# Performance work log

Hardware: AMD Instinct MI355X
Metric: run time of the kernel (lower is better)

Reference implementation:

```python
import jax, jax.numpy as jnp
import numpy as np

ALPHA = 0.1
B = 500_000
EMBED = 64
HIDDEN = 128
IN_DIM = 27 + 3 + EMBED  # 94

def _gelu(x):
    return jax.nn.gelu(x, approximate=False)  # torch.nn.GELU default = exact erf

def setup_inputs() -> dict:
    key = jax.random.key(0)
    ks = jax.random.split(key, 8)
    s = 0.05
    return {
        "F": jnp.eye(3, dtype=jnp.float32)[None] + 0.1 * jax.random.normal(ks[0], (B, 3, 3), jnp.float32),
        "latent_weight": jax.random.normal(ks[1], (1024, EMBED), jnp.float32),
        "W1": s * jax.random.normal(ks[2], (IN_DIM, HIDDEN), jnp.float32), "b1": jnp.zeros((HIDDEN,), jnp.float32),
        "W2": s * jax.random.normal(ks[3], (HIDDEN, HIDDEN), jnp.float32), "b2": jnp.zeros((HIDDEN,), jnp.float32),
        "W3": s * jax.random.normal(ks[4], (HIDDEN, HIDDEN), jnp.float32), "b3": jnp.zeros((HIDDEN,), jnp.float32),
        "W4": s * jax.random.normal(ks[5], (HIDDEN, HIDDEN), jnp.float32), "b4": jnp.zeros((HIDDEN,), jnp.float32),
        "W5": s * jax.random.normal(ks[6], (HIDDEN, 9), jnp.float32), "b5": jnp.zeros((9,), jnp.float32),
        "traj_ids": jnp.asarray(7, dtype=jnp.int32),
    }

def reference(F, latent_weight, W1, b1, W2, b2, W3, b3, W4, b4, W5, b5, traj_ids):
    n = F.shape[0]
    # Batched 3x3 SVD: F = U diag(s) Vh  (torch.svd returns V; Vh = V^T here)
    U, sigma, Vh = jnp.linalg.svd(F, full_matrices=False)
    R = jnp.matmul(U, Vh)  # [n,3,3] rotation
    lat = jnp.broadcast_to(latent_weight[traj_ids][None, :], (n, latent_weight.shape[1]))
    inv = jnp.concatenate(
        [F.reshape(n, 9), U.reshape(n, 9), sigma, Vh.reshape(n, 9), lat], axis=1)  # [n, 30+embed]
    h = _gelu(inv @ W1 + b1)
    h = _gelu(h @ W2 + b2)
    h = _gelu(h @ W3 + b3)
    h = _gelu(h @ W4 + b4)
    x = (h @ W5 + b5).reshape(n, 3, 3)
    x = 0.5 * (x + jnp.swapaxes(x, 1, 2))  # symmetrize
    return ALPHA * jnp.matmul(R, x) + F
```

## Files before the change

kernel.cpp:

```cpp
#include <hip/hip_runtime.h>


typedef short bf16x8 __attribute__((ext_vector_type(8)));
typedef float f32x4 __attribute__((ext_vector_type(4)));
typedef float f32x2 __attribute__((ext_vector_type(2)));
typedef unsigned int u32x2 __attribute__((ext_vector_type(2)));
typedef unsigned short u16;

#define WS_L1     0
#define WS_L234   8192
#define WS_L5     106496
#define WS_B1EFF  110592
#define WS_B234   111104
#define WS_B5     112640
#define WS_NEEDED 131072

__device__ __forceinline__ float bf2f(u16 b){
  union { unsigned int u; float f; } v; v.u = ((unsigned int)b) << 16; return v.f;
}
__device__ __forceinline__ u16 f2bf(float f){
  union { float f; unsigned int u; } v; v.f = f;
  unsigned int x = v.u;
  return (u16)((x + 0x7fffu + ((x >> 16) & 1u)) >> 16);
}
__device__ __forceinline__ unsigned int pack2bf(float f0, float f1){
  union { float f; unsigned int u; } a, b; a.f = f0; b.f = f1;
  unsigned int u0 = a.u + 0x8000u;
  unsigned int u1 = b.u + 0x8000u;
#if __has_builtin(__builtin_amdgcn_perm)
  return __builtin_amdgcn_perm(u1, u0, 0x07060302u);
#else
  return (u0 >> 16) | (u1 & 0xffff0000u);
#endif
}
template<bool B16>
__device__ __forceinline__ float ldf(const void* p, int i){
  return B16 ? bf2f(((const u16*)p)[i]) : ((const float*)p)[i];
}
template<bool B16>
__device__ __forceinline__ short ldw(const void* p, int i){
  return B16 ? (short)((const u16*)p)[i] : (short)f2bf(((const float*)p)[i]);
}
template<bool B16>
__device__ __forceinline__ void stf(void* p, int i, float v){
  if (B16) ((u16*)p)[i] = f2bf(v); else ((float*)p)[i] = v;
}

__device__ __forceinline__ float med3f(float x, float lo, float hi){
#if __has_builtin(__builtin_amdgcn_fmed3f)
  return __builtin_amdgcn_fmed3f(x, lo, hi);
#else
  return fminf(fmaxf(x, lo), hi);
#endif
}

__device__ __forceinline__ unsigned int gelu2_pack(float x0, float x1){
  const f32x2 A7 = {-2.20713e-4f, -2.20713e-4f};
  const f32x2 A5 = { 5.86695e-3f,  5.86695e-3f};
  const f32x2 A3 = {-5.99485e-2f, -5.99485e-2f};
  const f32x2 A1 = { 3.969014e-1f, 3.969014e-1f};
  const f32x2 HF = { 0.5f, 0.5f};
  f32x2 xc; xc[0] = med3f(x0, -3.4f, 3.4f); xc[1] = med3f(x1, -3.4f, 3.4f);
  f32x2 s  = xc * xc;
  f32x2 g  = s * A7 + A5;
  g = s * g + A3;
  g = s * g + A1;
  f32x2 ph = xc * g + HF;
  f32x2 xin; xin[0] = x0; xin[1] = x1;
  f32x2 y = xin * ph;
  return pack2bf(y[0], y[1]);
}

__device__ __forceinline__ int sniff_bf16(const void* Fg){
  const u16* fu = (const u16*)Fg;
  int votes = 0;
  #pragma unroll
  for (int k = 0; k < 32; ++k){
    u16 h = fu[k*18];
    votes += (h >= 0x3E00 && h < 0x4000) ? 1 : 0;
  }
  return votes >= 16;
}

template<int P, int Q, int R3>
__device__ __forceinline__ void jrot(float bm[3][3], float v[3][3]){
  float bpq = bm[P][Q];
  if (fabsf(bpq) < 1e-30f) return;
  float th = (bm[Q][Q] - bm[P][P]) / (2.0f * bpq);
  float t = copysignf(1.0f, th) / (fabsf(th) + sqrtf(1.0f + th*th));
  float c = 1.0f / sqrtf(1.0f + t*t);
  float s = t * c;
  float bpp = bm[P][P] - t*bpq;
  float bqq = bm[Q][Q] + t*bpq;
  bm[P][P] = bpp; bm[Q][Q] = bqq; bm[P][Q] = 0.0f; bm[Q][P] = 0.0f;
  float bpr = bm[P][R3], bqr = bm[Q][R3];
  float npr = c*bpr - s*bqr;
  float nqr = s*bpr + c*bqr;
  bm[P][R3] = npr; bm[R3][P] = npr;
  bm[Q][R3] = nqr; bm[R3][Q] = nqr;
  #pragma unroll
  for (int i = 0; i < 3; ++i){
    float vp = v[i][P], vq = v[i][Q];
    v[i][P] = c*vp - s*vq;
    v[i][Q] = s*vp + c*vq;
  }
}

__device__ __forceinline__ void svd3(const float Fm[9],
                                     float u[3][3], float sg[3], float vt[3][3]){
  float bm[3][3];
  #pragma unroll
  for (int i = 0; i < 3; ++i)
    #pragma unroll
    for (int j = i; j < 3; ++j){
      float acc = Fm[0*3+i]*Fm[0*3+j] + Fm[1*3+i]*Fm[1*3+j] + Fm[2*3+i]*Fm[2*3+j];
      bm[i][j] = acc; bm[j][i] = acc;
    }
  float v[3][3] = {{1.f,0.f,0.f},{0.f,1.f,0.f},{0.f,0.f,1.f}};
  #pragma unroll
  for (int sweep = 0; sweep < 5; ++sweep){
    jrot<0,1,2>(bm, v);
    jrot<0,2,1>(bm, v);
    jrot<1,2,0>(bm, v);
  }
  float lam0 = bm[0][0], lam1 = bm[1][1], lam2 = bm[2][2];
  #define CSWAP(la, lb, A, Bc) if ((la) < (lb)) { float t_ = la; la = lb; lb = t_; \
    for (int i_ = 0; i_ < 3; ++i_){ float w_ = v[i_][A]; v[i_][A] = v[i_][Bc]; v[i_][Bc] = w_; } }
  CSWAP(lam0, lam1, 0, 1);
  CSWAP(lam0, lam2, 0, 2);
  CSWAP(lam1, lam2, 1, 2);
  #undef CSWAP
  float a[3][3];
  #pragma unroll
  for (int c = 0; c < 3; ++c)
    #pragma unroll
    for (int r = 0; r < 3; ++r)
      a[r][c] = Fm[r*3+0]*v[0][c] + Fm[r*3+1]*v[1][c] + Fm[r*3+2]*v[2][c];
  float s1 = sqrtf(a[0][0]*a[0][0] + a[1][0]*a[1][0] + a[2][0]*a[2][0]);
  float inv1 = 1.0f / fmaxf(s1, 1e-30f);
  u[0][0] = a[0][0]*inv1; u[1][0] = a[1][0]*inv1; u[2][0] = a[2][0]*inv1;
  float d12 = u[0][0]*a[0][1] + u[1][0]*a[1][1] + u[2][0]*a[2][1];
  float w20 = a[0][1] - d12*u[0][0], w21 = a[1][1] - d12*u[1][0], w22 = a[2][1] - d12*u[2][0];
  float s2 = sqrtf(w20*w20 + w21*w21 + w22*w22);
  float inv2 = 1.0f / fmaxf(s2, 1e-30f);
  u[0][1] = w20*inv2; u[1][1] = w21*inv2; u[2][1] = w22*inv2;
  float d13 = u[0][0]*a[0][2] + u[1][0]*a[1][2] + u[2][0]*a[2][2];
  float d23 = u[0][1]*a[0][2] + u[1][1]*a[1][2] + u[2][1]*a[2][2];
  float w30 = a[0][2] - d13*u[0][0] - d23*u[0][1];
  float w31 = a[1][2] - d13*u[1][0] - d23*u[1][1];
  float w32 = a[2][2] - d13*u[2][0] - d23*u[2][1];
  float s3 = sqrtf(w30*w30 + w31*w31 + w32*w32);
  if (s3 > 1e-12f){
    float inv3 = 1.0f / s3;
    u[0][2] = w30*inv3; u[1][2] = w31*inv3; u[2][2] = w32*inv3;
  } else {
    float c0 = u[1][0]*u[2][1] - u[2][0]*u[1][1];
    float c1 = u[2][0]*u[0][1] - u[0][0]*u[2][1];
    float c2 = u[0][0]*u[1][1] - u[1][0]*u[0][1];
    float dt = c0*a[0][2] + c1*a[1][2] + c2*a[2][2];
    float sgn = (dt < 0.0f) ? -1.0f : 1.0f;
    u[0][2] = c0*sgn; u[1][2] = c1*sgn; u[2][2] = c2*sgn;
    s3 = fabsf(dt);
  }
  sg[0] = s1; sg[1] = s2; sg[2] = s3;
  #pragma unroll
  for (int i = 0; i < 3; ++i)
    #pragma unroll
    for (int j = 0; j < 3; ++j)
      vt[i][j] = v[j][i];
}

template<bool B16>
__device__ void prep_body(
  const void* latg, const void* w1g, const void* b1g,
  const void* w2g, const void* b2g, const void* w3g, const void* b3g,
  const void* w4g, const void* b4g, const void* w5g, const void* b5g,
  const int* trajg, char* ws)
{
  const int tid = threadIdx.x, lane = tid & 63, wv = tid >> 6;
  const int quad = lane >> 4, l15 = lane & 15;
  const int blk = blockIdx.x;
  if (blk < 27){
    const int wr = blk*4 + wv;
    bf16x8 frag;
    if (wr < 8){
      const int ntg = wr;
      #pragma unroll
      for (int j = 0; j < 8; ++j)
        frag[j] = ldw<B16>(w1g, (quad*8 + j)*128 + ntg*16 + l15);
      *(bf16x8*)(ws + WS_L1 + (size_t)(wr*64 + lane)*16) = frag;
    } else if (wr < 104){
      const int idx = wr - 8, layer = idx >> 5, rem = idx & 31;
      const int ntg = rem >> 2, ks = rem & 3;
      const void* wg = (layer == 0) ? w2g : ((layer == 1) ? w3g : w4g);
      #pragma unroll
      for (int j = 0; j < 8; ++j)
        frag[j] = ldw<B16>(wg, (ks*32 + quad*8 + j)*128 + ntg*16 + l15);
      *(bf16x8*)(ws + WS_L234 + (size_t)(idx*64 + lane)*16) = frag;
    } else {
      const int ks = wr - 104;
      #pragma unroll
      for (int j = 0; j < 8; ++j)
        frag[j] = (l15 < 9) ? ldw<B16>(w5g, (ks*32 + quad*8 + j)*9 + l15) : (short)0;
      *(bf16x8*)(ws + WS_L5 + (size_t)(ks*64 + lane)*16) = frag;
    }
  } else {
    if (tid < 128){
      const int t7 = trajg[0];
      float acc = ldf<B16>(b1g, tid);
      for (int j = 0; j < 64; ++j)
        acc += ldf<B16>(latg, t7*64 + j) * ldf<B16>(w1g, (30 + j)*128 + tid);
      ((float*)(ws + WS_B1EFF))[tid] = acc;
    } else {
      const int n = tid - 128;
      ((float*)(ws + WS_B234))[0*128 + n] = ldf<B16>(b2g, n);
      ((float*)(ws + WS_B234))[1*128 + n] = ldf<B16>(b3g, n);
      ((float*)(ws + WS_B234))[2*128 + n] = ldf<B16>(b4g, n);
      if (n < 16) ((float*)(ws + WS_B5))[n] = (n < 9) ? ldf<B16>(b5g, n) : 0.0f;
    }
  }
}

__global__ __launch_bounds__(256)
void fproj_prep_kernel(
  const void* Fg, const void* latg, const void* w1g, const void* b1g,
  const void* w2g, const void* b2g, const void* w3g, const void* b3g,
  const void* w4g, const void* b4g, const void* w5g, const void* b5g,
  const int* __restrict__ trajg, char* ws)
{
  if (sniff_bf16(Fg))
    prep_body<true >(latg, w1g, b1g, w2g, b2g, w3g, b3g, w4g, b4g, w5g, b5g, trajg, ws);
  else
    prep_body<false>(latg, w1g, b1g, w2g, b2g, w3g, b3g, w4g, b4g, w5g, b5g, trajg, ws);
}

union ShA { u16 X0[128][40]; float Xout[128][16]; };

template<bool B16, bool WS>
__device__ __forceinline__ void mlp_layer128(
    u16 (&Hbuf)[128][136],
    const void* __restrict__ Wg, const void* __restrict__ bg,
    const char* __restrict__ wsW, const float* __restrict__ bf32,
    int wv, int lane)
{
  const int l15  = lane & 15;
  const int quad = lane >> 4;
  const int kb   = quad * 8;
  f32x4 bb[2];
  #pragma unroll
  for (int nt = 0; nt < 2; ++nt){
    const int n0 = wv*32 + nt*16 + quad*4;
    if (WS) bb[nt] = *(const f32x4*)(bf32 + n0);
    else { bb[nt][0]=ldf<B16>(bg,n0); bb[nt][1]=ldf<B16>(bg,n0+1);
           bb[nt][2]=ldf<B16>(bg,n0+2); bb[nt][3]=ldf<B16>(bg,n0+3); }
  }
  bf16x8 Wf[2][4];
  #pragma unroll
  for (int nt = 0; nt < 2; ++nt){
    const int ntg = wv*2 + nt;
    #pragma unroll
    for (int ks = 0; ks < 4; ++ks){
      if (WS){
        Wf[nt][ks] = *(const bf16x8*)(wsW + (size_t)((ntg*4 + ks)*64 + lane)*16);
      } else {
        bf16x8 bv;
        #pragma unroll
        for (int j = 0; j < 8; ++j)
          bv[j] = ldw<B16>(Wg, (ks*32 + kb + j)*128 + ntg*16 + l15);
        Wf[nt][ks] = bv;
      }
    }
  }
  f32x4 acc[8][2];
  #pragma unroll
  for (int mt = 0; mt < 8; ++mt){
    const u16* hp = &Hbuf[mt*16 + l15][kb];
    bf16x8 a0 = *(const bf16x8*)(hp);
    bf16x8 a1 = *(const bf16x8*)(hp + 32);
    bf16x8 a2 = *(const bf16x8*)(hp + 64);
    bf16x8 a3 = *(const bf16x8*)(hp + 96);
    #pragma unroll
    for (int nt = 0; nt < 2; ++nt){
      f32x4 c = bb[nt];
      c = __builtin_amdgcn_mfma_f32_16x16x32_bf16(Wf[nt][0], a0, c, 0,0,0);
      c = __builtin_amdgcn_mfma_f32_16x16x32_bf16(Wf[nt][1], a1, c, 0,0,0);
      c = __builtin_amdgcn_mfma_f32_16x16x32_bf16(Wf[nt][2], a2, c, 0,0,0);
      c = __builtin_amdgcn_mfma_f32_16x16x32_bf16(Wf[nt][3], a3, c, 0,0,0);
      acc[mt][nt] = c;
    }
  }
  __syncthreads();
  #pragma unroll
  for (int nt = 0; nt < 2; ++nt){
    const int n0 = wv*32 + nt*16 + quad*4;
    #pragma unroll
    for (int mt = 0; mt < 8; ++mt){
      f32x4 c = acc[mt][nt];
      u32x2 pk;
      pk[0] = gelu2_pack(c[0], c[1]);
      pk[1] = gelu2_pack(c[2], c[3]);
      *(u32x2*)&Hbuf[mt*16 + l15][n0] = pk;
    }
  }
  __syncthreads();
}

template<bool B16, bool WS>
__device__ void fproj_body(
  const void* Fg, const void* latg,
  const void* w1g, const void* b1g, const void* w2g, const void* b2g,
  const void* w3g, const void* b3g, const void* w4g, const void* b4g,
  const void* w5g, const void* b5g,
  const int* trajg, void* outg, int ntot, const char* ws,
  ShA& shA, u16 (&Hbuf)[128][136], float* b1lds)
{
  const int tid  = threadIdx.x;
  const int lane = tid & 63;
  const int wv   = tid >> 6;
  const int l15  = lane & 15;
  const int quad = lane >> 4;
  const int kb   = quad * 8;
  const int row0 = blockIdx.x * 128;

  float Freg[9];
  float Rm[3][3];

  bf16x8 Wf1[2];
  #pragma unroll
  for (int nt = 0; nt < 2; ++nt){
    const int ntg = wv*2 + nt;
    if (WS){
      Wf1[nt] = *(const bf16x8*)(ws + WS_L1 + (size_t)(ntg*64 + lane)*16);
    } else {
      bf16x8 bv;
      #pragma unroll
      for (int j = 0; j < 8; ++j)
        bv[j] = ldw<B16>(w1g, (kb + j)*128 + ntg*16 + l15);
      Wf1[nt] = bv;
    }
  }

  if (tid < 128){
    const int r = row0 + tid;
    float fv[32];
    if (r < ntot){
      float A0[9];
      #pragma unroll
      for (int k = 0; k < 9; ++k){ A0[k] = ldf<B16>(Fg, r*9 + k); Freg[k] = A0[k]; }
      float uu[3][3], ss[3], vvt[3][3];
      svd3(A0, uu, ss, vvt);
      #pragma unroll
      for (int i = 0; i < 3; ++i)
        #pragma unroll
        for (int j = 0; j < 3; ++j)
          Rm[i][j] = uu[i][0]*vvt[0][j] + uu[i][1]*vvt[1][j] + uu[i][2]*vvt[2][j];
      #pragma unroll
      for (int k = 0; k < 9; ++k) fv[k]    = A0[k];
      #pragma unroll
      for (int k = 0; k < 9; ++k) fv[9+k]  = uu[k/3][k%3];
      fv[18] = ss[0]; fv[19] = ss[1]; fv[20] = ss[2];
      #pragma unroll
      for (int k = 0; k < 9; ++k) fv[21+k] = vvt[k/3][k%3];
      fv[30] = 0.0f; fv[31] = 0.0f;
    } else {
      #pragma unroll
      for (int k = 0; k < 32; ++k) fv[k] = 0.0f;
      #pragma unroll
      for (int k = 0; k < 9; ++k) Freg[k] = 0.0f;
      #pragma unroll
      for (int i = 0; i < 3; ++i)
        #pragma unroll
        for (int j = 0; j < 3; ++j) Rm[i][j] = 0.0f;
    }
    #pragma unroll
    for (int q = 0; q < 4; ++q){
      u32x2 pk;
      pk[0] = pack2bf(fv[q*8+0], fv[q*8+1]);
      pk[1] = pack2bf(fv[q*8+2], fv[q*8+3]);
      *(u32x2*)&shA.X0[tid][q*8 + 0] = pk;
      pk[0] = pack2bf(fv[q*8+4], fv[q*8+5]);
      pk[1] = pack2bf(fv[q*8+6], fv[q*8+7]);
      *(u32x2*)&shA.X0[tid][q*8 + 4] = pk;
    }
  } else if (!WS){
    const int n = tid - 128;
    const int t7 = trajg[0];
    float acc = ldf<B16>(b1g, n);
    for (int j = 0; j < 64; ++j)
      acc += ldf<B16>(latg, t7*64 + j) * ldf<B16>(w1g, (30 + j)*128 + n);
    b1lds[n] = acc;
  }
  __syncthreads();

  {
    f32x4 bb[2];
    #pragma unroll
    for (int nt = 0; nt < 2; ++nt){
      const int n0 = wv*32 + nt*16 + quad*4;
      if (WS) bb[nt] = *(const f32x4*)((const float*)(ws + WS_B1EFF) + n0);
      else { bb[nt][0]=b1lds[n0]; bb[nt][1]=b1lds[n0+1]; bb[nt][2]=b1lds[n0+2]; bb[nt][3]=b1lds[n0+3]; }
    }
    f32x4 acc[8][2];
    #pragma unroll
    for (int mt = 0; mt < 8; ++mt){
      bf16x8 av = *(const bf16x8*)&shA.X0[mt*16 + l15][kb];
      #pragma unroll
      for (int nt = 0; nt < 2; ++nt){
        f32x4 c = bb[nt];
        c = __builtin_amdgcn_mfma_f32_16x16x32_bf16(Wf1[nt], av, c, 0,0,0);
        acc[mt][nt] = c;
      }
    }
    __syncthreads();
    #pragma unroll
    for (int nt = 0; nt < 2; ++nt){
      const int n0 = wv*32 + nt*16 + quad*4;
      #pragma unroll
      for (int mt = 0; mt < 8; ++mt){
        f32x4 c = acc[mt][nt];
        u32x2 pk;
        pk[0] = gelu2_pack(c[0], c[1]);
        pk[1] = gelu2_pack(c[2], c[3]);
        *(u32x2*)&Hbuf[mt*16 + l15][n0] = pk;
      }
    }
  }
  __syncthreads();

  const float* bf32 = (const float*)(ws + WS_B234);
  mlp_layer128<B16,WS>(Hbuf, w2g, b2g, ws + WS_L234 + 0*32768, bf32 + 0*128, wv, lane);
  mlp_layer128<B16,WS>(Hbuf, w3g, b3g, ws + WS_L234 + 1*32768, bf32 + 1*128, wv, lane);
  mlp_layer128<B16,WS>(Hbuf, w4g, b4g, ws + WS_L234 + 2*32768, bf32 + 2*128, wv, lane);

  {
    bf16x8 W5f[4];
    #pragma unroll
    for (int ks = 0; ks < 4; ++ks){
      if (WS){
        W5f[ks] = *(const bf16x8*)(ws + WS_L5 + (size_t)(ks*64 + lane)*16);
      } else {
        bf16x8 bv;
        #pragma unroll
        for (int j = 0; j < 8; ++j)
          bv[j] = (l15 < 9) ? ldw<B16>(w5g, (ks*32 + kb + j)*9 + l15) : (short)0;
        W5f[ks] = bv;
      }
    }
    f32x4 bb5;
    if (WS) bb5 = *(const f32x4*)((const float*)(ws + WS_B5) + quad*4);
    else {
      #pragma unroll
      for (int rg = 0; rg < 4; ++rg)
        bb5[rg] = (quad*4 + rg < 9) ? ldf<B16>(b5g, quad*4 + rg) : 0.0f;
    }
    #pragma unroll
    for (int t = 0; t < 2; ++t){
      const int mt = wv*2 + t;
      const u16* hp = &Hbuf[mt*16 + l15][kb];
      bf16x8 a0 = *(const bf16x8*)(hp);
      bf16x8 a1 = *(const bf16x8*)(hp + 32);
      bf16x8 a2 = *(const bf16x8*)(hp + 64);
      bf16x8 a3 = *(const bf16x8*)(hp + 96);
      f32x4 c = bb5;
      c = __builtin_amdgcn_mfma_f32_16x16x32_bf16(W5f[0], a0, c, 0,0,0);
      c = __builtin_amdgcn_mfma_f32_16x16x32_bf16(W5f[1], a1, c, 0,0,0);
      c = __builtin_amdgcn_mfma_f32_16x16x32_bf16(W5f[2], a2, c, 0,0,0);
      c = __builtin_amdgcn_mfma_f32_16x16x32_bf16(W5f[3], a3, c, 0,0,0);
      *(f32x4*)&shA.Xout[mt*16 + l15][quad*4] = c;
    }
  }
  __syncthreads();

  if (tid < 128){
    const int r = row0 + tid;
    if (r < ntot){
      float x[9];
      #pragma unroll
      for (int k = 0; k < 9; ++k) x[k] = shA.Xout[tid][k];
      float xs[3][3];
      #pragma unroll
      for (int i = 0; i < 3; ++i)
        #pragma unroll
        for (int j = 0; j < 3; ++j)
          xs[i][j] = 0.5f*(x[i*3+j] + x[j*3+i]);
      #pragma unroll
      for (int i = 0; i < 3; ++i)
        #pragma unroll
        for (int j = 0; j < 3; ++j){
          float y = Rm[i][0]*xs[0][j] + Rm[i][1]*xs[1][j] + Rm[i][2]*xs[2][j];
          stf<B16>(outg, r*9 + i*3 + j, 0.1f*y + Freg[i*3+j]);
        }
    }
  }
}

__global__ __launch_bounds__(256, 3)
void fproj_ws_kernel(
  const void* Fg, const void* latg,
  const void* w1g, const void* b1g, const void* w2g, const void* b2g,
  const void* w3g, const void* b3g, const void* w4g, const void* b4g,
  const void* w5g, const void* b5g,
  const int* __restrict__ trajg, void* outg, int ntot, const char* ws)
{
  __shared__ ShA shA;
  __shared__ alignas(16) u16 Hbuf[128][136];
  if (sniff_bf16(Fg))
    fproj_body<true , true>(Fg, latg, w1g, b1g, w2g, b2g, w3g, b3g, w4g, b4g,
                            w5g, b5g, trajg, outg, ntot, ws, shA, Hbuf, nullptr);
  else
    fproj_body<false, true>(Fg, latg, w1g, b1g, w2g, b2g, w3g, b3g, w4g, b4g,
                            w5g, b5g, trajg, outg, ntot, ws, shA, Hbuf, nullptr);
}

__global__ __launch_bounds__(256, 3)
void fproj_plain_kernel(
  const void* Fg, const void* latg,
  const void* w1g, const void* b1g, const void* w2g, const void* b2g,
  const void* w3g, const void* b3g, const void* w4g, const void* b4g,
  const void* w5g, const void* b5g,
  const int* __restrict__ trajg, void* outg, int ntot)
{
  __shared__ ShA shA;
  __shared__ alignas(16) u16 Hbuf[128][136];
  __shared__ float b1lds[128];
  if (sniff_bf16(Fg))
    fproj_body<true , false>(Fg, latg, w1g, b1g, w2g, b2g, w3g, b3g, w4g, b4g,
                             w5g, b5g, trajg, outg, ntot, nullptr, shA, Hbuf, b1lds);
  else
    fproj_body<false, false>(Fg, latg, w1g, b1g, w2g, b2g, w3g, b3g, w4g, b4g,
                             w5g, b5g, trajg, outg, ntot, nullptr, shA, Hbuf, b1lds);
}

extern "C" void kernel_launch(void* const* d_in, const int* in_sizes, int n_in,
                              void* d_out, int out_size, void* d_ws, size_t ws_size,
                              hipStream_t stream) {
  (void)n_in; (void)out_size;
  const int n = in_sizes[0] / 9;
  dim3 grid((n + 127) / 128), block(256);
  if (ws_size >= (size_t)WS_NEEDED){
    hipLaunchKernelGGL(fproj_prep_kernel, dim3(28), block, 0, stream,
      (const void*)d_in[0],  (const void*)d_in[1],
      (const void*)d_in[2],  (const void*)d_in[3],
      (const void*)d_in[4],  (const void*)d_in[5],
      (const void*)d_in[6],  (const void*)d_in[7],
      (const void*)d_in[8],  (const void*)d_in[9],
      (const void*)d_in[10], (const void*)d_in[11],
      (const int*)d_in[12], (char*)d_ws);
    hipLaunchKernelGGL(fproj_ws_kernel, grid, block, 0, stream,
      (const void*)d_in[0],  (const void*)d_in[1],
      (const void*)d_in[2],  (const void*)d_in[3],
      (const void*)d_in[4],  (const void*)d_in[5],
      (const void*)d_in[6],  (const void*)d_in[7],
      (const void*)d_in[8],  (const void*)d_in[9],
      (const void*)d_in[10], (const void*)d_in[11],
      (const int*)d_in[12], d_out, n, (const char*)d_ws);
  } else {
    hipLaunchKernelGGL(fproj_plain_kernel, grid, block, 0, stream,
      (const void*)d_in[0],  (const void*)d_in[1],
      (const void*)d_in[2],  (const void*)d_in[3],
      (const void*)d_in[4],  (const void*)d_in[5],
      (const void*)d_in[6],  (const void*)d_in[7],
      (const void*)d_in[8],  (const void*)d_in[9],
      (const void*)d_in[10], (const void*)d_in[11],
      (const int*)d_in[12], d_out, n);
  }
}
```

Baseline: 199.5 us.

## Give each wave a private row stripe to drop per-layer block barriers

```diff
diff --git a/kernel.cpp b/kernel.cpp
--- a/kernel.cpp
+++ b/kernel.cpp
@@ -234,75 +234,55 @@
     prep_body<false>(latg, w1g, b1g, w2g, b2g, w3g, b3g, w4g, b4g, w5g, b5g, trajg, ws);
 }
 
-union ShA { u16 X0[128][40]; float Xout[128][16]; };
-
 template<bool B16, bool WS>
-__device__ __forceinline__ void mlp_layer128(
-    u16 (&Hbuf)[128][136],
+__device__ __forceinline__ void mlp_layer_stripe(
+    u16 (&Hbuf)[128][136], int wrow, int lane,
     const void* __restrict__ Wg, const void* __restrict__ bg,
-    const char* __restrict__ wsW, const float* __restrict__ bf32,
-    int wv, int lane)
+    const char* __restrict__ wsW, const float* __restrict__ bf32)
 {
-  const int l15  = lane & 15;
-  const int quad = lane >> 4;
-  const int kb   = quad * 8;
-  f32x4 bb[2];
-  #pragma unroll
-  for (int nt = 0; nt < 2; ++nt){
-    const int n0 = wv*32 + nt*16 + quad*4;
-    if (WS) bb[nt] = *(const f32x4*)(bf32 + n0);
-    else { bb[nt][0]=ldf<B16>(bg,n0); bb[nt][1]=ldf<B16>(bg,n0+1);
-           bb[nt][2]=ldf<B16>(bg,n0+2); bb[nt][3]=ldf<B16>(bg,n0+3); }
-  }
-  bf16x8 Wf[2][4];
-  #pragma unroll
-  for (int nt = 0; nt < 2; ++nt){
-    const int ntg = wv*2 + nt;
-    #pragma unroll
-    for (int ks = 0; ks < 4; ++ks){
-      if (WS){
-        Wf[nt][ks] = *(const bf16x8*)(wsW + (size_t)((ntg*4 + ks)*64 + lane)*16);
-      } else {
+  const int l15 = lane & 15, quad = lane >> 4, kb = quad*8;
+  f32x4 acc[2][8];
+  #pragma unroll
+  for (int ntg = 0; ntg < 8; ++ntg){
+    const int n0 = ntg*16 + quad*4;
+    f32x4 bb;
+    if (WS) bb = *(const f32x4*)(bf32 + n0);
+    else { bb[0]=ldf<B16>(bg,n0); bb[1]=ldf<B16>(bg,n0+1);
+           bb[2]=ldf<B16>(bg,n0+2); bb[3]=ldf<B16>(bg,n0+3); }
+    acc[0][ntg] = bb; acc[1][ntg] = bb;
+  }
+  #pragma unroll
+  for (int ks = 0; ks < 4; ++ks){
+    bf16x8 Af[8];
+    #pragma unroll
+    for (int ntg = 0; ntg < 8; ++ntg){
+      if (WS) Af[ntg] = *(const bf16x8*)(wsW + (size_t)((ntg*4 + ks)*64 + lane)*16);
+      else {
         bf16x8 bv;
         #pragma unroll
         for (int j = 0; j < 8; ++j)
           bv[j] = ldw<B16>(Wg, (ks*32 + kb + j)*128 + ntg*16 + l15);
-        Wf[nt][ks] = bv;
+        Af[ntg] = bv;
       }
     }
-  }
-  f32x4 acc[8][2];
-  #pragma unroll
-  for (int mt = 0; mt < 8; ++mt){
-    const u16* hp = &Hbuf[mt*16 + l15][kb];
-    bf16x8 a0 = *(const bf16x8*)(hp);
-    bf16x8 a1 = *(const bf16x8*)(hp + 32);
-    bf16x8 a2 = *(const bf16x8*)(hp + 64);
-    bf16x8 a3 = *(const bf16x8*)(hp + 96);
-    #pragma unroll
-    for (int nt = 0; nt < 2; ++nt){
-      f32x4 c = bb[nt];
-      c = __builtin_amdgcn_mfma_f32_16x16x32_bf16(Wf[nt][0], a0, c, 0,0,0);
-      c = __builtin_amdgcn_mfma_f32_16x16x32_bf16(Wf[nt][1], a1, c, 0,0,0);
-      c = __builtin_amdgcn_mfma_f32_16x16x32_bf16(Wf[nt][2], a2, c, 0,0,0);
-      c = __builtin_amdgcn_mfma_f32_16x16x32_bf16(Wf[nt][3], a3, c, 0,0,0);
-      acc[mt][nt] = c;
-    }
-  }
-  __syncthreads();
-  #pragma unroll
-  for (int nt = 0; nt < 2; ++nt){
-    const int n0 = wv*32 + nt*16 + quad*4;
-    #pragma unroll
-    for (int mt = 0; mt < 8; ++mt){
-      f32x4 c = acc[mt][nt];
+    #pragma unroll
+    for (int mt = 0; mt < 2; ++mt){
+      bf16x8 bfrag = *(const bf16x8*)&Hbuf[wrow + mt*16 + l15][ks*32 + kb];
+      #pragma unroll
+      for (int ntg = 0; ntg < 8; ++ntg)
+        acc[mt][ntg] = __builtin_amdgcn_mfma_f32_16x16x32_bf16(Af[ntg], bfrag, acc[mt][ntg], 0,0,0);
+    }
+  }
+  #pragma unroll
+  for (int mt = 0; mt < 2; ++mt)
+    #pragma unroll
+    for (int ntg = 0; ntg < 8; ++ntg){
+      f32x4 c = acc[mt][ntg];
       u32x2 pk;
       pk[0] = gelu2_pack(c[0], c[1]);
       pk[1] = gelu2_pack(c[2], c[3]);
-      *(u32x2*)&Hbuf[mt*16 + l15][n0] = pk;
-    }
-  }
-  __syncthreads();
+      *(u32x2*)&Hbuf[wrow + mt*16 + l15][ntg*16 + quad*4] = pk;
+    }
 }
 
 template<bool B16, bool WS>
@@ -312,7 +292,7 @@
   const void* w3g, const void* b3g, const void* w4g, const void* b4g,
   const void* w5g, const void* b5g,
   const int* trajg, void* outg, int ntot, const char* ws,
-  ShA& shA, u16 (&Hbuf)[128][136], float* b1lds)
+  u16 (&Hbuf)[128][136], float* b1lds)
 {
   const int tid  = threadIdx.x;
   const int lane = tid & 63;
@@ -320,25 +300,11 @@
   const int l15  = lane & 15;
   const int quad = lane >> 4;
   const int kb   = quad * 8;
+  const int wrow = wv * 32;
   const int row0 = blockIdx.x * 128;
 
   float Freg[9];
   float Rm[3][3];
-
-  bf16x8 Wf1[2];
-  #pragma unroll
-  for (int nt = 0; nt < 2; ++nt){
-    const int ntg = wv*2 + nt;
-    if (WS){
-      Wf1[nt] = *(const bf16x8*)(ws + WS_L1 + (size_t)(ntg*64 + lane)*16);
-    } else {
-      bf16x8 bv;
-      #pragma unroll
-      for (int j = 0; j < 8; ++j)
-        bv[j] = ldw<B16>(w1g, (kb + j)*128 + ntg*16 + l15);
-      Wf1[nt] = bv;
-    }
-  }
 
   if (tid < 128){
     const int r = row0 + tid;
@@ -377,10 +343,10 @@
       u32x2 pk;
       pk[0] = pack2bf(fv[q*8+0], fv[q*8+1]);
       pk[1] = pack2bf(fv[q*8+2], fv[q*8+3]);
-      *(u32x2*)&shA.X0[tid][q*8 + 0] = pk;
+      *(u32x2*)&Hbuf[tid][q*8 + 0] = pk;
       pk[0] = pack2bf(fv[q*8+4], fv[q*8+5]);
       pk[1] = pack2bf(fv[q*8+6], fv[q*8+7]);
-      *(u32x2*)&shA.X0[tid][q*8 + 4] = pk;
+      *(u32x2*)&Hbuf[tid][q*8 + 4] = pk;
     }
   } else if (!WS){
     const int n = tid - 128;
@@ -393,90 +359,93 @@
   __syncthreads();
 
   {
-    f32x4 bb[2];
-    #pragma unroll
-    for (int nt = 0; nt < 2; ++nt){
-      const int n0 = wv*32 + nt*16 + quad*4;
-      if (WS) bb[nt] = *(const f32x4*)((const float*)(ws + WS_B1EFF) + n0);
-      else { bb[nt][0]=b1lds[n0]; bb[nt][1]=b1lds[n0+1]; bb[nt][2]=b1lds[n0+2]; bb[nt][3]=b1lds[n0+3]; }
-    }
-    f32x4 acc[8][2];
-    #pragma unroll
-    for (int mt = 0; mt < 8; ++mt){
-      bf16x8 av = *(const bf16x8*)&shA.X0[mt*16 + l15][kb];
-      #pragma unroll
-      for (int nt = 0; nt < 2; ++nt){
-        f32x4 c = bb[nt];
-        c = __builtin_amdgcn_mfma_f32_16x16x32_bf16(Wf1[nt], av, c, 0,0,0);
-        acc[mt][nt] = c;
+    f32x4 acc[2][8];
+    #pragma unroll
+    for (int ntg = 0; ntg < 8; ++ntg){
+      const int n0 = ntg*16 + quad*4;
+      f32x4 bb;
+      if (WS) bb = *(const f32x4*)((const float*)(ws + WS_B1EFF) + n0);
+      else { bb[0]=b1lds[n0]; bb[1]=b1lds[n0+1]; bb[2]=b1lds[n0+2]; bb[3]=b1lds[n0+3]; }
+      acc[0][ntg] = bb; acc[1][ntg] = bb;
+    }
+    bf16x8 Af[8];
+    #pragma unroll
+    for (int ntg = 0; ntg < 8; ++ntg){
+      if (WS) Af[ntg] = *(const bf16x8*)(ws + WS_L1 + (size_t)(ntg*64 + lane)*16);
+      else {
+        bf16x8 bv;
+        #pragma unroll
+        for (int j = 0; j < 8; ++j)
+          bv[j] = ldw<B16>(w1g, (kb + j)*128 + ntg*16 + l15);
+        Af[ntg] = bv;
       }
     }
-    __syncthreads();
-    #pragma unroll
-    for (int nt = 0; nt < 2; ++nt){
-      const int n0 = wv*32 + nt*16 + quad*4;
-      #pragma unroll
-      for (int mt = 0; mt < 8; ++mt){
-        f32x4 c = acc[mt][nt];
+    #pragma unroll
+    for (int mt = 0; mt < 2; ++mt){
+      bf16x8 bfrag = *(const bf16x8*)&Hbuf[wrow + mt*16 + l15][kb];
+      #pragma unroll
+      for (int ntg = 0; ntg < 8; ++ntg)
+        acc[mt][ntg] = __builtin_amdgcn_mfma_f32_16x16x32_bf16(Af[ntg], bfrag, acc[mt][ntg], 0,0,0);
+    }
+    #pragma unroll
+    for (int mt = 0; mt < 2; ++mt)
+      #pragma unroll
+      for (int ntg = 0; ntg < 8; ++ntg){
+        f32x4 c = acc[mt][ntg];
         u32x2 pk;
         pk[0] = gelu2_pack(c[0], c[1]);
         pk[1] = gelu2_pack(c[2], c[3]);
-        *(u32x2*)&Hbuf[mt*16 + l15][n0] = pk;
+        *(u32x2*)&Hbuf[wrow + mt*16 + l15][ntg*16 + quad*4] = pk;
       }
-    }
-  }
-  __syncthreads();
+  }
 
   const float* bf32 = (const float*)(ws + WS_B234);
-  mlp_layer128<B16,WS>(Hbuf, w2g, b2g, ws + WS_L234 + 0*32768, bf32 + 0*128, wv, lane);
-  mlp_layer128<B16,WS>(Hbuf, w3g, b3g, ws + WS_L234 + 1*32768, bf32 + 1*128, wv, lane);
-  mlp_layer128<B16,WS>(Hbuf, w4g, b4g, ws + WS_L234 + 2*32768, bf32 + 2*128, wv, lane);
+  mlp_layer_stripe<B16,WS>(Hbuf, wrow, lane, w2g, b2g, ws + WS_L234 + 0*32768, bf32 + 0*128);
+  mlp_layer_stripe<B16,WS>(Hbuf, wrow, lane, w3g, b3g, ws + WS_L234 + 1*32768, bf32 + 1*128);
+  mlp_layer_stripe<B16,WS>(Hbuf, wrow, lane, w4g, b4g, ws + WS_L234 + 2*32768, bf32 + 2*128);
 
   {
-    bf16x8 W5f[4];
+    f32x4 acc5[2];
+    {
+      f32x4 bb5;
+      if (WS) bb5 = *(const f32x4*)((const float*)(ws + WS_B5) + quad*4);
+      else {
+        #pragma unroll
+        for (int rg = 0; rg < 4; ++rg)
+          bb5[rg] = (quad*4 + rg < 9) ? ldf<B16>(b5g, quad*4 + rg) : 0.0f;
+      }
+      acc5[0] = bb5; acc5[1] = bb5;
+    }
     #pragma unroll
     for (int ks = 0; ks < 4; ++ks){
-      if (WS){
-        W5f[ks] = *(const bf16x8*)(ws + WS_L5 + (size_t)(ks*64 + lane)*16);
-      } else {
+      bf16x8 W5f;
+      if (WS) W5f = *(const bf16x8*)(ws + WS_L5 + (size_t)(ks*64 + lane)*16);
+      else {
         bf16x8 bv;
         #pragma unroll
         for (int j = 0; j < 8; ++j)
           bv[j] = (l15 < 9) ? ldw<B16>(w5g, (ks*32 + kb + j)*9 + l15) : (short)0;
-        W5f[ks] = bv;
+        W5f = bv;
       }
-    }
-    f32x4 bb5;
-    if (WS) bb5 = *(const f32x4*)((const float*)(ws + WS_B5) + quad*4);
-    else {
-      #pragma unroll
-      for (int rg = 0; rg < 4; ++rg)
-        bb5[rg] = (quad*4 + rg < 9) ? ldf<B16>(b5g, quad*4 + rg) : 0.0f;
-    }
-    #pragma unroll
-    for (int t = 0; t < 2; ++t){
-      const int mt = wv*2 + t;
-      const u16* hp = &Hbuf[mt*16 + l15][kb];
-      bf16x8 a0 = *(const bf16x8*)(hp);
-      bf16x8 a1 = *(const bf16x8*)(hp + 32);
-      bf16x8 a2 = *(const bf16x8*)(hp + 64);
-      bf16x8 a3 = *(const bf16x8*)(hp + 96);
-      f32x4 c = bb5;
-      c = __builtin_amdgcn_mfma_f32_16x16x32_bf16(W5f[0], a0, c, 0,0,0);
-      c = __builtin_amdgcn_mfma_f32_16x16x32_bf16(W5f[1], a1, c, 0,0,0);
-      c = __builtin_amdgcn_mfma_f32_16x16x32_bf16(W5f[2], a2, c, 0,0,0);
-      c = __builtin_amdgcn_mfma_f32_16x16x32_bf16(W5f[3], a3, c, 0,0,0);
-      *(f32x4*)&shA.Xout[mt*16 + l15][quad*4] = c;
-    }
+      #pragma unroll
+      for (int mt = 0; mt < 2; ++mt){
+        bf16x8 bfrag = *(const bf16x8*)&Hbuf[wrow + mt*16 + l15][ks*32 + kb];
+        acc5[mt] = __builtin_amdgcn_mfma_f32_16x16x32_bf16(W5f, bfrag, acc5[mt], 0,0,0);
+      }
+    }
+    #pragma unroll
+    for (int mt = 0; mt < 2; ++mt)
+      *(f32x4*)((float*)&Hbuf[wrow + mt*16 + l15][0] + quad*4) = acc5[mt];
   }
   __syncthreads();
 
   if (tid < 128){
     const int r = row0 + tid;
     if (r < ntot){
+      const float* xr = (const float*)&Hbuf[tid][0];
       float x[9];
       #pragma unroll
-      for (int k = 0; k < 9; ++k) x[k] = shA.Xout[tid][k];
+      for (int k = 0; k < 9; ++k) x[k] = xr[k];
       float xs[3][3];
       #pragma unroll
       for (int i = 0; i < 3; ++i)
@@ -502,14 +471,13 @@
   const void* w5g, const void* b5g,
   const int* __restrict__ trajg, void* outg, int ntot, const char* ws)
 {
-  __shared__ ShA shA;
   __shared__ alignas(16) u16 Hbuf[128][136];
   if (sniff_bf16(Fg))
     fproj_body<true , true>(Fg, latg, w1g, b1g, w2g, b2g, w3g, b3g, w4g, b4g,
-                            w5g, b5g, trajg, outg, ntot, ws, shA, Hbuf, nullptr);
+                            w5g, b5g, trajg, outg, ntot, ws, Hbuf, nullptr);
   else
     fproj_body<false, true>(Fg, latg, w1g, b1g, w2g, b2g, w3g, b3g, w4g, b4g,
-                            w5g, b5g, trajg, outg, ntot, ws, shA, Hbuf, nullptr);
+                            w5g, b5g, trajg, outg, ntot, ws, Hbuf, nullptr);
 }
 
 __global__ __launch_bounds__(256, 3)
@@ -520,15 +488,14 @@
   const void* w5g, const void* b5g,
   const int* __restrict__ trajg, void* outg, int ntot)
 {
-  __shared__ ShA shA;
   __shared__ alignas(16) u16 Hbuf[128][136];
   __shared__ float b1lds[128];
   if (sniff_bf16(Fg))
     fproj_body<true , false>(Fg, latg, w1g, b1g, w2g, b2g, w3g, b3g, w4g, b4g,
-                             w5g, b5g, trajg, outg, ntot, nullptr, shA, Hbuf, b1lds);
+                             w5g, b5g, trajg, outg, ntot, nullptr, Hbuf, b1lds);
   else
     fproj_body<false, false>(Fg, latg, w1g, b1g, w2g, b2g, w3g, b3g, w4g, b4g,
-                             w5g, b5g, trajg, outg, ntot, nullptr, shA, Hbuf, b1lds);
+                             w5g, b5g, trajg, outg, ntot, nullptr, Hbuf, b1lds);
 }
 
 extern "C" void kernel_launch(void* const* d_in, const int* in_sizes, int n_in,
```

Result: slower. 212.5 us (+6.5%).
